# Kernel optimization log

Hardware: AMD Instinct MI355X
Metric: run time of the kernel (lower is better)

The kernel has to match this reference:

```python
import math
import jax, jax.numpy as jnp
import numpy as np

B, L, D = 64, 1024, 64

def setup_inputs() -> dict:
    key = jax.random.key(0)
    k1, k2, k3, k4, k5, k6 = jax.random.split(key, 6)
    return {
        "queries": jax.random.normal(k1, (B, L, D), dtype=jnp.float32),
        "keys": jax.random.normal(k2, (B, L, D), dtype=jnp.float32),
        "values": jax.random.normal(k3, (B, L, D), dtype=jnp.float32),
        "pos_k": jax.random.normal(k4, (L, L, D), dtype=jnp.float32),
        "pos_v": jax.random.normal(k5, (L, L, D), dtype=jnp.float32),
        "valid_lens": jax.random.randint(k6, (B,), 0, L, dtype=jnp.int32),
    }

MASK_VALUE = -1e6  # matches torch source's -1000000.0 fill

def reference(queries, keys, values, pos_k, pos_v, valid_lens):
    d = queries.shape[-1]
    scale = 1.0 / math.sqrt(d)
    # content scores: [B, Lq, Lk]
    scores = jnp.einsum("bqd,bkd->bqk", queries, keys)
    # relative-position scores: contract each query position with its RPR key table
    scores_pos = jnp.einsum("bqd,qkd->bqk", queries, pos_k)
    scores = (scores + scores_pos) * scale
    # mask keys beyond valid_lens[b] with -1e6 (as in sequence_mask), then softmax
    kpos = jnp.arange(scores.shape[-1])
    mask = kpos[None, None, :] < valid_lens[:, None, None]  # [B,1,Lk] -> broadcast
    scores = jnp.where(mask, scores, MASK_VALUE)
    attn = jax.nn.softmax(scores, axis=-1)  # [B, Lq, Lk]
    # dropout prob = 0.0 -> identity
    out = jnp.einsum("bqk,bkd->bqd", attn, values)
    out_pos = jnp.einsum("bqk,qkd->bqd", attn, pos_v)
    return out + out_pos
```

## Files before the change

### kernel.cpp

```cpp
#include <hip/hip_runtime.h>
#include <hip/hip_bf16.h>

typedef __attribute__((ext_vector_type(8))) short bf16x8;
typedef __attribute__((ext_vector_type(4))) float f32x4;

#define B_SZ 64
#define L_SZ 1024
#define D_SZ 64
#define SCALE 0.125f

#define KP 36
#define BPITCH 580
#define SA_SZ 9280

__device__ __forceinline__ short f2bf(float f) {
    union { float f; unsigned u; } v; v.f = f;
    unsigned r = (v.u + 0x7fffu + ((v.u >> 16) & 1u)) >> 16;
    return (short)r;
}

__device__ __forceinline__ bf16x8 cvt8(const float* __restrict__ p) {
    f32x4 a = *(const f32x4*)p;
    f32x4 b = *(const f32x4*)(p + 4);
    bf16x8 r;
    r[0] = f2bf(a[0]); r[1] = f2bf(a[1]); r[2] = f2bf(a[2]); r[3] = f2bf(a[3]);
    r[4] = f2bf(b[0]); r[5] = f2bf(b[1]); r[6] = f2bf(b[2]); r[7] = f2bf(b[3]);
    return r;
}

#define MFMA(A, Bf, C) __builtin_amdgcn_mfma_f32_16x16x32_bf16(A, Bf, C, 0, 0, 0)

__global__ __launch_bounds__(512, 2) void rpr_attn(
    const float* __restrict__ Q, const float* __restrict__ Kt,
    const float* __restrict__ V, const float* __restrict__ PK,
    const float* __restrict__ PV, const int* __restrict__ VLEN,
    float* __restrict__ OUT)
{
    __shared__ float SA[2][SA_SZ];
    __shared__ float lbuf[2][256];

    const int tid = threadIdx.x;
    const int wave = tid >> 6, lane = tid & 63;
    const int g = wave >> 2, r = wave & 3;
    const int lane15 = lane & 15, quad = lane >> 4;
    const int b0 = blockIdx.x * 16;
    const int q0 = blockIdx.y * 16;

    float* sa = SA[g];

    bf16x8 qa[4][2], qp[4][2];
    int vl[4];
#pragma unroll
    for (int j = 0; j < 4; ++j) {
        const int bl = r * 4 + j;
        vl[j] = VLEN[b0 + bl];
        const float* pc = Q + ((b0 + bl) * L_SZ + q0 + lane15) * D_SZ + quad * 8;
        qa[j][0] = cvt8(pc); qa[j][1] = cvt8(pc + 32);
        const float* pp = Q + ((b0 + lane15) * L_SZ + q0 + bl) * D_SZ + quad * 8;
        qp[j][0] = cvt8(pp); qp[j][1] = cvt8(pp + 32);
    }

    f32x4 Oc[4][4], Op[4][4];
#pragma unroll
    for (int j = 0; j < 4; ++j)
#pragma unroll
        for (int nt = 0; nt < 4; ++nt) {
            Oc[j][nt] = (f32x4){0.f, 0.f, 0.f, 0.f};
            Op[j][nt] = (f32x4){0.f, 0.f, 0.f, 0.f};
        }
    float l_acc = 0.f;

    const int tg = r * 64 + lane;
    const int lb = tg >> 4, lq = tg & 15;

    for (int it = 0; it < 16; ++it) {
        const int kb = g * 512 + it * 32;

#pragma unroll
        for (int j = 0; j < 4; ++j) {
            const int ql = r * 4 + j;
#pragma unroll
            for (int c = 0; c < 2; ++c) {
                const float* bp = PK + ((q0 + ql) * L_SZ + kb + c * 16 + lane15) * D_SZ + quad * 8;
                f32x4 acc = (f32x4){0.f, 0.f, 0.f, 0.f};
                acc = MFMA(qp[j][0], cvt8(bp), acc);
                acc = MFMA(qp[j][1], cvt8(bp + 32), acc);
#pragma unroll
                for (int i = 0; i < 4; ++i)
                    sa[(quad * 4 + i) * BPITCH + ql * KP + c * 16 + lane15] = acc[i];
            }
        }
        __syncthreads();

#pragma unroll
        for (int j = 0; j < 4; ++j) {
            const int bl = r * 4 + j;
#pragma unroll
            for (int c = 0; c < 2; ++c) {
                const float* bp = Kt + ((b0 + bl) * L_SZ + kb + c * 16 + lane15) * D_SZ + quad * 8;
                f32x4 acc = (f32x4){0.f, 0.f, 0.f, 0.f};
                acc = MFMA(qa[j][0], cvt8(bp), acc);
                acc = MFMA(qa[j][1], cvt8(bp + 32), acc);
                const int kg = kb + c * 16 + lane15;
#pragma unroll
                for (int i = 0; i < 4; ++i) {
                    const int idx = bl * BPITCH + (quad * 4 + i) * KP + c * 16 + lane15;
                    const float s = (acc[i] + sa[idx]) * SCALE;
                    float e;
                    if (vl[j] == 0)       e = 1.0f;
                    else if (kg < vl[j])  e = __expf(s);
                    else                  e = 0.0f;
                    sa[idx] = e;
                }
            }
        }
        __syncthreads();

        {
            const float* row = sa + lb * BPITCH + lq * KP;
            float s = 0.f;
#pragma unroll
            for (int kk = 0; kk < 32; kk += 4) {
                f32x4 v4 = *(const f32x4*)(row + kk);
                s += v4[0] + v4[1] + v4[2] + v4[3];
            }
            l_acc += s;
        }
#pragma unroll
        for (int j = 0; j < 4; ++j) {
            const int bl = r * 4 + j;
            const bf16x8 af = cvt8(sa + bl * BPITCH + lane15 * KP + quad * 8);
            const float* vb = V + ((b0 + bl) * L_SZ + kb + quad * 8) * D_SZ + lane15;
#pragma unroll
            for (int nt = 0; nt < 4; ++nt) {
                bf16x8 bf;
#pragma unroll
                for (int jj = 0; jj < 8; ++jj) bf[jj] = f2bf(vb[jj * D_SZ + nt * 16]);
                Oc[j][nt] = MFMA(af, bf, Oc[j][nt]);
            }
        }
#pragma unroll
        for (int j = 0; j < 4; ++j) {
            const int ql = r * 4 + j;
            const bf16x8 af = cvt8(sa + lane15 * BPITCH + ql * KP + quad * 8);
            const float* vb = PV + ((q0 + ql) * L_SZ + kb + quad * 8) * D_SZ + lane15;
#pragma unroll
            for (int nt = 0; nt < 4; ++nt) {
                bf16x8 bf;
#pragma unroll
                for (int jj = 0; jj < 8; ++jj) bf[jj] = f2bf(vb[jj * D_SZ + nt * 16]);
                Op[j][nt] = MFMA(af, bf, Op[j][nt]);
            }
        }
        __syncthreads();
    }

    lbuf[g][tg] = l_acc;
    float* Obuf = &SA[0][0];

    if (g == 0) {
#pragma unroll
        for (int j = 0; j < 4; ++j)
#pragma unroll
            for (int nt = 0; nt < 4; ++nt)
#pragma unroll
                for (int i = 0; i < 4; ++i)
                    Obuf[((r * 4 + j) * 16 + quad * 4 + i) * 64 + nt * 16 + lane15] = Oc[j][nt][i];
    }
    __syncthreads();
    if (g == 1) {
#pragma unroll
        for (int j = 0; j < 4; ++j)
#pragma unroll
            for (int nt = 0; nt < 4; ++nt)
#pragma unroll
                for (int i = 0; i < 4; ++i)
                    Obuf[((r * 4 + j) * 16 + quad * 4 + i) * 64 + nt * 16 + lane15] += Oc[j][nt][i];
    }
    __syncthreads();
    if (g == 0) {
#pragma unroll
        for (int j = 0; j < 4; ++j)
#pragma unroll
            for (int nt = 0; nt < 4; ++nt)
#pragma unroll
                for (int i = 0; i < 4; ++i)
                    Obuf[((quad * 4 + i) * 16 + r * 4 + j) * 64 + nt * 16 + lane15] += Op[j][nt][i];
    }
    __syncthreads();
    if (g == 1) {
#pragma unroll
        for (int j = 0; j < 4; ++j)
#pragma unroll
            for (int nt = 0; nt < 4; ++nt)
#pragma unroll
                for (int i = 0; i < 4; ++i)
                    Obuf[((quad * 4 + i) * 16 + r * 4 + j) * 64 + nt * 16 + lane15] += Op[j][nt][i];
    }
    __syncthreads();

    for (int idx = tid; idx < 4096; idx += 512) {
        const int d4 = idx & 15, ql2 = (idx >> 4) & 15, bl2 = idx >> 8;
        const float li = lbuf[0][bl2 * 16 + ql2] + lbuf[1][bl2 * 16 + ql2];
        const float rl = 1.0f / li;
        f32x4 o = *(const f32x4*)&Obuf[(bl2 * 16 + ql2) * 64 + d4 * 4];
        o[0] *= rl; o[1] *= rl; o[2] *= rl; o[3] *= rl;
        *(f32x4*)&OUT[((b0 + bl2) * L_SZ + q0 + ql2) * D_SZ + d4 * 4] = o;
    }
}

extern "C" void kernel_launch(void* const* d_in, const int* in_sizes, int n_in,
                              void* d_out, int out_size, void* d_ws, size_t ws_size,
                              hipStream_t stream) {
    (void)in_sizes; (void)n_in; (void)out_size; (void)d_ws; (void)ws_size;
    const float* Q  = (const float*)d_in[0];
    const float* K  = (const float*)d_in[1];
    const float* V  = (const float*)d_in[2];
    const float* PK = (const float*)d_in[3];
    const float* PV = (const float*)d_in[4];
    const int*   VL = (const int*)d_in[5];
    float* OUT = (float*)d_out;

    dim3 grid(4, 64, 1);
    dim3 block(512, 1, 1);
    rpr_attn<<<grid, block, 0, stream>>>(Q, K, V, PK, PV, VL, OUT);
}
```

Baseline: 1.019 ms.

## Split key range across blocks with atomic accumulation and pre-transposed bf16 V

Restructures the work split. Each block now covers 32 batches × 16 queries × 256 keys, so every PK/PV tile is reused across 32 batches instead of 16, which halves the reads of the large positional tables. Partial outputs and softmax denominators from the split key ranges are combined with global atomics into a zeroed workspace, and a separate kernel normalises the result. V is pre-transposed into bf16 so that its MFMA operand loads become single vector loads instead of strided scalar converts. The cost is three extra kernel launches, atomic traffic on a 16 MB buffer, and a block-index swizzle that keeps both batch halves adjacent for L2 reuse.

Result: slower. 1.634 ms (+60.3%).

```diff
diff --git a/kernel.cpp b/kernel.cpp
--- a/kernel.cpp
+++ b/kernel.cpp
@@ -4,14 +4,18 @@
 typedef __attribute__((ext_vector_type(8))) short bf16x8;
 typedef __attribute__((ext_vector_type(4))) float f32x4;
 
-#define B_SZ 64
 #define L_SZ 1024
 #define D_SZ 64
 #define SCALE 0.125f
 
 #define KP 36
-#define BPITCH 580
-#define SA_SZ 9280
+#define BP 580
+#define SA_F 18560
+#define OD 68
+
+#define OACC_BYTES 16777216
+#define LACC_BYTES 262144
+#define VT_OFF 17039360
 
 __device__ __forceinline__ short f2bf(float f) {
     union { float f; unsigned u; } v; v.f = f;
@@ -30,189 +34,231 @@
 
 #define MFMA(A, Bf, C) __builtin_amdgcn_mfma_f32_16x16x32_bf16(A, Bf, C, 0, 0, 0)
 
-__global__ __launch_bounds__(512, 2) void rpr_attn(
-    const float* __restrict__ Q, const float* __restrict__ Kt,
-    const float* __restrict__ V, const float* __restrict__ PK,
-    const float* __restrict__ PV, const int* __restrict__ VLEN,
-    float* __restrict__ OUT)
+__global__ void zero_ws(float* __restrict__ p, int n4) {
+    int i = blockIdx.x * 256 + threadIdx.x;
+    if (i < n4) ((f32x4*)p)[i] = (f32x4){0.f, 0.f, 0.f, 0.f};
+}
+
+__global__ void transpose_v(const float* __restrict__ V, unsigned short* __restrict__ Vt) {
+    __shared__ float T[64][65];
+    const int b = blockIdx.y, k0 = blockIdx.x * 64;
+    const int t = threadIdx.x;
+    {
+        const int kl = t >> 2, dq = (t & 3) * 16;
+        const float* src = V + (b * L_SZ + k0 + kl) * D_SZ + dq;
+#pragma unroll
+        for (int j = 0; j < 16; j += 4) {
+            f32x4 v = *(const f32x4*)(src + j);
+            T[kl][dq + j] = v[0]; T[kl][dq + j + 1] = v[1];
+            T[kl][dq + j + 2] = v[2]; T[kl][dq + j + 3] = v[3];
+        }
+    }
+    __syncthreads();
+    {
+        const int d = t >> 2, kq = (t & 3) * 16;
+        bf16x8 o0, o1;
+#pragma unroll
+        for (int j = 0; j < 8; ++j) o0[j] = f2bf(T[kq + j][d]);
+#pragma unroll
+        for (int j = 0; j < 8; ++j) o1[j] = f2bf(T[kq + 8 + j][d]);
+        unsigned short* dst = Vt + (b * D_SZ + d) * L_SZ + k0 + kq;
+        *(bf16x8*)dst = o0;
+        *(bf16x8*)(dst + 8) = o1;
+    }
+}
+
+__global__ __launch_bounds__(512, 2) void rpr_main(
+    const float* __restrict__ Q, const float* __restrict__ K,
+    const float* __restrict__ PK, const float* __restrict__ PV,
+    const int* __restrict__ VLEN, const unsigned short* __restrict__ Vt,
+    float* __restrict__ Oacc, float* __restrict__ Lacc)
 {
-    __shared__ float SA[2][SA_SZ];
-    __shared__ float lbuf[2][256];
-
+    __shared__ float SA[SA_F];
     const int tid = threadIdx.x;
     const int wave = tid >> 6, lane = tid & 63;
-    const int g = wave >> 2, r = wave & 3;
     const int lane15 = lane & 15, quad = lane >> 4;
-    const int b0 = blockIdx.x * 16;
-    const int q0 = blockIdx.y * 16;
-
-    float* sa = SA[g];
-
-    bf16x8 qa[4][2], qp[4][2];
+    const int id = blockIdx.x;
+    const int g = (id & 7) | ((id >> 4) << 3);
+    const int m = (id >> 3) & 1;
+    const int q0 = (g >> 2) << 4;
+    const int kbase = (g & 3) << 8;
+    const int b0 = m << 5;
+
+    bf16x8 qa[4][2];
     int vl[4];
 #pragma unroll
     for (int j = 0; j < 4; ++j) {
-        const int bl = r * 4 + j;
-        vl[j] = VLEN[b0 + bl];
-        const float* pc = Q + ((b0 + bl) * L_SZ + q0 + lane15) * D_SZ + quad * 8;
-        qa[j][0] = cvt8(pc); qa[j][1] = cvt8(pc + 32);
-        const float* pp = Q + ((b0 + lane15) * L_SZ + q0 + bl) * D_SZ + quad * 8;
-        qp[j][0] = cvt8(pp); qp[j][1] = cvt8(pp + 32);
-    }
-
-    f32x4 Oc[4][4], Op[4][4];
+        const int b = b0 + wave * 4 + j;
+        vl[j] = VLEN[b];
+        const float* p = Q + (b * L_SZ + q0 + lane15) * D_SZ + quad * 8;
+        qa[j][0] = cvt8(p); qa[j][1] = cvt8(p + 32);
+    }
+    bf16x8 qp[2][2][2];
+#pragma unroll
+    for (int j = 0; j < 2; ++j) {
+        const int q = q0 + wave * 2 + j;
+#pragma unroll
+        for (int mt = 0; mt < 2; ++mt) {
+            const float* p = Q + ((b0 + mt * 16 + lane15) * L_SZ + q) * D_SZ + quad * 8;
+            qp[j][mt][0] = cvt8(p); qp[j][mt][1] = cvt8(p + 32);
+        }
+    }
+
+    f32x4 Oc[4][4];
+    f32x4 Op[2][2][4];
 #pragma unroll
     for (int j = 0; j < 4; ++j)
 #pragma unroll
-        for (int nt = 0; nt < 4; ++nt) {
-            Oc[j][nt] = (f32x4){0.f, 0.f, 0.f, 0.f};
-            Op[j][nt] = (f32x4){0.f, 0.f, 0.f, 0.f};
-        }
+        for (int nt = 0; nt < 4; ++nt) Oc[j][nt] = (f32x4){0.f, 0.f, 0.f, 0.f};
+#pragma unroll
+    for (int j = 0; j < 2; ++j)
+#pragma unroll
+        for (int mt = 0; mt < 2; ++mt)
+#pragma unroll
+            for (int nt = 0; nt < 4; ++nt) Op[j][mt][nt] = (f32x4){0.f, 0.f, 0.f, 0.f};
     float l_acc = 0.f;
-
-    const int tg = r * 64 + lane;
-    const int lb = tg >> 4, lq = tg & 15;
-
-    for (int it = 0; it < 16; ++it) {
-        const int kb = g * 512 + it * 32;
+    const int row_b = tid >> 4, row_q = tid & 15;
+
+    for (int it = 0; it < 8; ++it) {
+        const int kb = kbase + it * 32;
+
+#pragma unroll
+        for (int j = 0; j < 2; ++j) {
+            const int ql = wave * 2 + j;
+            const int q = q0 + ql;
+#pragma unroll
+            for (int nt = 0; nt < 2; ++nt) {
+                const float* bp = PK + (q * L_SZ + kb + nt * 16 + lane15) * D_SZ + quad * 8;
+                bf16x8 f0 = cvt8(bp), f1 = cvt8(bp + 32);
+#pragma unroll
+                for (int mt = 0; mt < 2; ++mt) {
+                    f32x4 acc = (f32x4){0.f, 0.f, 0.f, 0.f};
+                    acc = MFMA(qp[j][mt][0], f0, acc);
+                    acc = MFMA(qp[j][mt][1], f1, acc);
+                    const int base = (mt * 16 + quad * 4) * BP + ql * KP + nt * 16 + lane15;
+#pragma unroll
+                    for (int i = 0; i < 4; ++i) SA[base + i * BP] = acc[i];
+                }
+            }
+        }
+        __syncthreads();
 
 #pragma unroll
         for (int j = 0; j < 4; ++j) {
-            const int ql = r * 4 + j;
-#pragma unroll
-            for (int c = 0; c < 2; ++c) {
-                const float* bp = PK + ((q0 + ql) * L_SZ + kb + c * 16 + lane15) * D_SZ + quad * 8;
-                f32x4 acc = (f32x4){0.f, 0.f, 0.f, 0.f};
-                acc = MFMA(qp[j][0], cvt8(bp), acc);
-                acc = MFMA(qp[j][1], cvt8(bp + 32), acc);
-#pragma unroll
-                for (int i = 0; i < 4; ++i)
-                    sa[(quad * 4 + i) * BPITCH + ql * KP + c * 16 + lane15] = acc[i];
-            }
-        }
-        __syncthreads();
-
-#pragma unroll
-        for (int j = 0; j < 4; ++j) {
-            const int bl = r * 4 + j;
-#pragma unroll
-            for (int c = 0; c < 2; ++c) {
-                const float* bp = Kt + ((b0 + bl) * L_SZ + kb + c * 16 + lane15) * D_SZ + quad * 8;
+            const int bl = wave * 4 + j;
+            const int b = b0 + bl;
+#pragma unroll
+            for (int nt = 0; nt < 2; ++nt) {
+                const float* bp = K + (b * L_SZ + kb + nt * 16 + lane15) * D_SZ + quad * 8;
                 f32x4 acc = (f32x4){0.f, 0.f, 0.f, 0.f};
                 acc = MFMA(qa[j][0], cvt8(bp), acc);
                 acc = MFMA(qa[j][1], cvt8(bp + 32), acc);
-                const int kg = kb + c * 16 + lane15;
+                const int kg = kb + nt * 16 + lane15;
+                const int base = bl * BP + quad * 4 * KP + nt * 16 + lane15;
 #pragma unroll
                 for (int i = 0; i < 4; ++i) {
-                    const int idx = bl * BPITCH + (quad * 4 + i) * KP + c * 16 + lane15;
-                    const float s = (acc[i] + sa[idx]) * SCALE;
+                    const int idx = base + i * KP;
+                    const float s = (acc[i] + SA[idx]) * SCALE;
                     float e;
-                    if (vl[j] == 0)       e = 1.0f;
-                    else if (kg < vl[j])  e = __expf(s);
-                    else                  e = 0.0f;
-                    sa[idx] = e;
+                    if (vl[j] == 0)      e = 1.0f;
+                    else if (kg < vl[j]) e = __expf(s);
+                    else                 e = 0.0f;
+                    SA[idx] = e;
                 }
             }
         }
         __syncthreads();
 
         {
-            const float* row = sa + lb * BPITCH + lq * KP;
+            const float* row = SA + row_b * BP + row_q * KP;
             float s = 0.f;
 #pragma unroll
             for (int kk = 0; kk < 32; kk += 4) {
-                f32x4 v4 = *(const f32x4*)(row + kk);
-                s += v4[0] + v4[1] + v4[2] + v4[3];
+                f32x4 v = *(const f32x4*)(row + kk);
+                s += v[0] + v[1] + v[2] + v[3];
             }
             l_acc += s;
         }
 #pragma unroll
         for (int j = 0; j < 4; ++j) {
-            const int bl = r * 4 + j;
-            const bf16x8 af = cvt8(sa + bl * BPITCH + lane15 * KP + quad * 8);
-            const float* vb = V + ((b0 + bl) * L_SZ + kb + quad * 8) * D_SZ + lane15;
+            const int bl = wave * 4 + j;
+            const int b = b0 + bl;
+            const bf16x8 af = cvt8(SA + bl * BP + lane15 * KP + quad * 8);
+#pragma unroll
+            for (int nt = 0; nt < 4; ++nt) {
+                const bf16x8 bf = *(const bf16x8*)(Vt + (b * D_SZ + nt * 16 + lane15) * L_SZ + kb + quad * 8);
+                Oc[j][nt] = MFMA(af, bf, Oc[j][nt]);
+            }
+        }
+#pragma unroll
+        for (int j = 0; j < 2; ++j) {
+            const int ql = wave * 2 + j;
+            const int q = q0 + ql;
+            const bf16x8 a0 = cvt8(SA + lane15 * BP + ql * KP + quad * 8);
+            const bf16x8 a1 = cvt8(SA + (16 + lane15) * BP + ql * KP + quad * 8);
+            const float* pvb = PV + (q * L_SZ + kb + quad * 8) * D_SZ + lane15;
 #pragma unroll
             for (int nt = 0; nt < 4; ++nt) {
                 bf16x8 bf;
 #pragma unroll
-                for (int jj = 0; jj < 8; ++jj) bf[jj] = f2bf(vb[jj * D_SZ + nt * 16]);
-                Oc[j][nt] = MFMA(af, bf, Oc[j][nt]);
-            }
-        }
-#pragma unroll
-        for (int j = 0; j < 4; ++j) {
-            const int ql = r * 4 + j;
-            const bf16x8 af = cvt8(sa + lane15 * BPITCH + ql * KP + quad * 8);
-            const float* vb = PV + ((q0 + ql) * L_SZ + kb + quad * 8) * D_SZ + lane15;
-#pragma unroll
-            for (int nt = 0; nt < 4; ++nt) {
-                bf16x8 bf;
-#pragma unroll
-                for (int jj = 0; jj < 8; ++jj) bf[jj] = f2bf(vb[jj * D_SZ + nt * 16]);
-                Op[j][nt] = MFMA(af, bf, Op[j][nt]);
-            }
-        }
-        __syncthreads();
-    }
-
-    lbuf[g][tg] = l_acc;
-    float* Obuf = &SA[0][0];
-
-    if (g == 0) {
-#pragma unroll
-        for (int j = 0; j < 4; ++j)
+                for (int jj = 0; jj < 8; ++jj) bf[jj] = f2bf(pvb[jj * D_SZ + nt * 16]);
+                Op[j][0][nt] = MFMA(a0, bf, Op[j][0][nt]);
+                Op[j][1][nt] = MFMA(a1, bf, Op[j][1][nt]);
+            }
+        }
+        __syncthreads();
+    }
+
+    float* Ob = SA;
+#pragma unroll
+    for (int h = 0; h < 2; ++h) {
+        if ((wave >> 2) == h) {
+#pragma unroll
+            for (int j = 0; j < 4; ++j) {
+                const int ob = (wave & 3) * 4 + j;
+#pragma unroll
+                for (int nt = 0; nt < 4; ++nt)
+#pragma unroll
+                    for (int i = 0; i < 4; ++i)
+                        Ob[ob * (16 * OD) + (quad * 4 + i) * OD + nt * 16 + lane15] = Oc[j][nt][i];
+            }
+        }
+        __syncthreads();
+#pragma unroll
+        for (int j = 0; j < 2; ++j) {
+            const int ql = wave * 2 + j;
 #pragma unroll
             for (int nt = 0; nt < 4; ++nt)
 #pragma unroll
                 for (int i = 0; i < 4; ++i)
-                    Obuf[((r * 4 + j) * 16 + quad * 4 + i) * 64 + nt * 16 + lane15] = Oc[j][nt][i];
-    }
-    __syncthreads();
-    if (g == 1) {
-#pragma unroll
-        for (int j = 0; j < 4; ++j)
-#pragma unroll
-            for (int nt = 0; nt < 4; ++nt)
-#pragma unroll
-                for (int i = 0; i < 4; ++i)
-                    Obuf[((r * 4 + j) * 16 + quad * 4 + i) * 64 + nt * 16 + lane15] += Oc[j][nt][i];
-    }
-    __syncthreads();
-    if (g == 0) {
-#pragma unroll
-        for (int j = 0; j < 4; ++j)
-#pragma unroll
-            for (int nt = 0; nt < 4; ++nt)
-#pragma unroll
-                for (int i = 0; i < 4; ++i)
-                    Obuf[((quad * 4 + i) * 16 + r * 4 + j) * 64 + nt * 16 + lane15] += Op[j][nt][i];
-    }
-    __syncthreads();
-    if (g == 1) {
-#pragma unroll
-        for (int j = 0; j < 4; ++j)
-#pragma unroll
-            for (int nt = 0; nt < 4; ++nt)
-#pragma unroll
-                for (int i = 0; i < 4; ++i)
-                    Obuf[((quad * 4 + i) * 16 + r * 4 + j) * 64 + nt * 16 + lane15] += Op[j][nt][i];
-    }
-    __syncthreads();
-
-    for (int idx = tid; idx < 4096; idx += 512) {
-        const int d4 = idx & 15, ql2 = (idx >> 4) & 15, bl2 = idx >> 8;
-        const float li = lbuf[0][bl2 * 16 + ql2] + lbuf[1][bl2 * 16 + ql2];
-        const float rl = 1.0f / li;
-        f32x4 o = *(const f32x4*)&Obuf[(bl2 * 16 + ql2) * 64 + d4 * 4];
-        o[0] *= rl; o[1] *= rl; o[2] *= rl; o[3] *= rl;
-        *(f32x4*)&OUT[((b0 + bl2) * L_SZ + q0 + ql2) * D_SZ + d4 * 4] = o;
-    }
+                    Ob[(quad * 4 + i) * (16 * OD) + ql * OD + nt * 16 + lane15] += Op[j][h][nt][i];
+        }
+        __syncthreads();
+        {
+            const int pair = tid >> 1, ob = pair >> 4, oq = pair & 15, ds = (tid & 1) * 32;
+            float* dst = Oacc + ((b0 + h * 16 + ob) * L_SZ + q0 + oq) * D_SZ + ds;
+            const float* srcp = Ob + ob * (16 * OD) + oq * OD + ds;
+#pragma unroll
+            for (int dd = 0; dd < 32; ++dd) atomicAdd(dst + dd, srcp[dd]);
+        }
+        __syncthreads();
+    }
+    atomicAdd(&Lacc[(b0 + row_b) * L_SZ + q0 + row_q], l_acc);
+}
+
+__global__ void norm_out(const float* __restrict__ Oacc, const float* __restrict__ Lacc,
+                         float* __restrict__ OUT) {
+    const int i4 = blockIdx.x * 256 + threadIdx.x;
+    f32x4 o = ((const f32x4*)Oacc)[i4];
+    const float rl = 1.0f / Lacc[i4 >> 4];
+    o[0] *= rl; o[1] *= rl; o[2] *= rl; o[3] *= rl;
+    ((f32x4*)OUT)[i4] = o;
 }
 
 extern "C" void kernel_launch(void* const* d_in, const int* in_sizes, int n_in,
                               void* d_out, int out_size, void* d_ws, size_t ws_size,
                               hipStream_t stream) {
-    (void)in_sizes; (void)n_in; (void)out_size; (void)d_ws; (void)ws_size;
+    (void)in_sizes; (void)n_in; (void)out_size; (void)ws_size;
     const float* Q  = (const float*)d_in[0];
     const float* K  = (const float*)d_in[1];
     const float* V  = (const float*)d_in[2];
@@ -221,7 +267,12 @@
     const int*   VL = (const int*)d_in[5];
     float* OUT = (float*)d_out;
 
-    dim3 grid(4, 64, 1);
-    dim3 block(512, 1, 1);
-    rpr_attn<<<grid, block, 0, stream>>>(Q, K, V, PK, PV, VL, OUT);
-}
+    float* Oacc = (float*)d_ws;
+    float* Lacc = (float*)((char*)d_ws + OACC_BYTES);
+    unsigned short* Vt = (unsigned short*)((char*)d_ws + VT_OFF);
+
+    zero_ws<<<4160, 256, 0, stream>>>((float*)d_ws, (OACC_BYTES + LACC_BYTES) / 16);
+    transpose_v<<<dim3(16, 64), 256, 0, stream>>>(V, Vt);
+    rpr_main<<<512, 512, 0, stream>>>(Q, K, PK, PV, VL, Vt, Oacc, Lacc);
+    norm_out<<<4096, 256, 0, stream>>>(Oacc, Lacc, OUT);
+}
```
